# Kernel tuning notes

Hardware: AMD Instinct MI355X
Metric: run time of the kernel (lower is better)

Reference implementation:

```python
import jax, jax.numpy as jnp
import numpy as np

NEG_SLOPE = 0.2
EPS = 1e-16


def gat_layer(x, edge_index, edge_attr, W, We, a_src, a_dst, a_edge, bias,
              add_self_loops):
    """PyG GATConv with concat=True.
    x: [N, F_in], edge_index: [2, E] (row 0 = src j, row 1 = dst i),
    edge_attr: [E, De], W: [F_in, H*C], We: [De, H*C],
    a_src/a_dst/a_edge: [H, C], bias: [H*C].
    """
    N = x.shape[0]
    H, C = a_src.shape
    if add_self_loops:
        # fill_value='mean': self-loop edge_attr = mean of incoming edge_attr per node
        dst0 = edge_index[1]
        s = jax.ops.segment_sum(edge_attr, dst0, num_segments=N)
        cnt = jax.ops.segment_sum(jnp.ones((edge_attr.shape[0], 1), edge_attr.dtype),
                                  dst0, num_segments=N)
        loop_attr = s / jnp.maximum(cnt, 1.0)
        loop_idx = jnp.arange(N, dtype=edge_index.dtype)
        edge_index = jnp.concatenate(
            [edge_index, jnp.stack([loop_idx, loop_idx])], axis=1)
        edge_attr = jnp.concatenate([edge_attr, loop_attr], axis=0)

    src, dst = edge_index[0], edge_index[1]
    h = (x @ W).reshape(N, H, C)                       # [N, H, C]
    e = (edge_attr @ We).reshape(-1, H, C)             # [E, H, C]

    alpha_src = jnp.einsum('nhc,hc->nh', h, a_src)     # [N, H]
    alpha_dst = jnp.einsum('nhc,hc->nh', h, a_dst)     # [N, H]
    alpha_edge = jnp.einsum('ehc,hc->eh', e, a_edge)   # [E, H]

    alpha = alpha_src[src] + alpha_dst[dst] + alpha_edge
    alpha = jax.nn.leaky_relu(alpha, NEG_SLOPE)

    # segment softmax over destination node
    amax = jax.ops.segment_max(alpha, dst, num_segments=N)      # [N, H]
    ex = jnp.exp(alpha - amax[dst])
    denom = jax.ops.segment_sum(ex, dst, num_segments=N)        # [N, H]
    attn = ex / (denom[dst] + EPS)                               # [E, H]

    msg = h[src] * attn[:, :, None]                              # [E, H, C]
    out = jax.ops.segment_sum(msg, dst, num_segments=N)          # [N, H, C]
    return out.reshape(N, H * C) + bias


def setup_inputs() -> dict:
    key = jax.random.key(0)
    ks = jax.random.split(key, 16)
    N, E, F_in, C, H, De = 10000, 160000, 128, 64, 8, 1
    d1 = H * C  # 512

    def glorot(k, shape):
        fan = shape[0] + shape[-1]
        s = jnp.sqrt(6.0 / fan)
        return jax.random.uniform(k, shape, jnp.float32, -s, s)

    return {
        'x': jax.random.normal(ks[0], (N, F_in), jnp.float32),
        'edge_index': jax.random.randint(ks[1], (2, E), 0, N, jnp.int32),
        'edge_attr': jax.random.normal(ks[2], (E, De), jnp.float32),
        # layer 1 params
        'W1': glorot(ks[3], (F_in, d1)),
        'We1': glorot(ks[4], (De, d1)),
        'as1': glorot(ks[5], (H, C)),
        'ad1': glorot(ks[6], (H, C)),
        'ae1': glorot(ks[7], (H, C)),
        'b1': jnp.zeros((d1,), jnp.float32),
        # layer 2 params
        'W2': glorot(ks[8], (d1, d1)),
        'We2': glorot(ks[9], (De, d1)),
        'as2': glorot(ks[10], (H, C)),
        'ad2': glorot(ks[11], (H, C)),
        'ae2': glorot(ks[12], (H, C)),
        'b2': jnp.zeros((d1,), jnp.float32),
    }


def reference(x, edge_index, edge_attr,
              W1, We1, as1, ad1, ae1, b1,
              W2, We2, as2, ad2, ae2, b2):
    h = gat_layer(x, edge_index, edge_attr, W1, We1, as1, ad1, ae1, b1,
                  add_self_loops=False)
    h = jax.nn.relu(h)
    h = gat_layer(h, edge_index, edge_attr, W2, We2, as2, ad2, ae2, b2,
                  add_self_loops=True)
    return jnp.mean(h, axis=0)  # [512]
```

## Files before the change

kernel.cpp:

```cpp
#include <hip/hip_runtime.h>
#include <hip/hip_bf16.h>

#define HD __device__ __forceinline__
typedef unsigned short u16;
typedef __attribute__((ext_vector_type(8))) short bf16x8;
typedef __attribute__((ext_vector_type(4))) float f32x4;

HD u16 f2b(float f){
  unsigned u = __float_as_uint(f);
  unsigned r = (u + 0x7fffu + ((u>>16)&1u)) >> 16;
  return (u16)r;
}
HD float b2f(short s){ return __uint_as_float(((unsigned)(u16)s)<<16); }

__global__ void k_count(const int* __restrict__ dst, const float* __restrict__ ea,
                        int* cnt, float* easum, int E){
  int e = blockIdx.x*blockDim.x + threadIdx.x;
  if (e>=E) return;
  int d = dst[e];
  atomicAdd(&cnt[d],1);
  atomicAdd(&easum[d], ea[e]);
}

__global__ __launch_bounds__(1024) void k_scan(const int* __restrict__ cnt, int* offs, int N){
  __shared__ int lds[1024];
  const int chunk = (N + 1023)/1024;
  const int b = threadIdx.x*chunk;
  int s = 0;
  for (int i=0;i<chunk;++i){ int idx=b+i; if (idx<N) s += cnt[idx]; }
  lds[threadIdx.x] = s;
  __syncthreads();
  #pragma unroll
  for (int off=1; off<1024; off<<=1){
    int t = (threadIdx.x>=(unsigned)off)? lds[threadIdx.x-off] : 0;
    __syncthreads();
    lds[threadIdx.x] += t;
    __syncthreads();
  }
  int excl = lds[threadIdx.x] - s;
  for (int i=0;i<chunk;++i){
    int idx=b+i;
    if (idx<N){ offs[idx] = excl; excl += cnt[idx]; }
  }
  if (threadIdx.x==1023) offs[N] = lds[1023];
}

__global__ void k_scatter(const int* __restrict__ src, const int* __restrict__ dst,
                          const float* __restrict__ ea, const int* __restrict__ offs,
                          int* fill, int* srcs, float* eas, int E){
  int e = blockIdx.x*blockDim.x + threadIdx.x;
  if (e>=E) return;
  int d = dst[e];
  int p = offs[d] + atomicAdd(&fill[d],1);
  srcs[p] = src[e];
  eas[p]  = ea[e];
}

__global__ __launch_bounds__(512) void k_prep_small(
    const int* __restrict__ cnt, const float* __restrict__ easum, float* la, int N,
    const float* __restrict__ We1, const float* __restrict__ ae1,
    const float* __restrict__ We2, const float* __restrict__ ae2,
    float* wedot, int nbLoop){
  int bx = blockIdx.x;
  if (bx < nbLoop){
    int n = bx*512 + threadIdx.x;
    if (n<N) la[n] = easum[n] / fmaxf((float)cnt[n], 1.f);
    return;
  }
  int which = bx - nbLoop;
  const float* We = which? We2 : We1;
  const float* ae = which? ae2 : ae1;
  int hh = threadIdx.x>>6, lane = threadIdx.x&63;
  float p = We[hh*64+lane]*ae[hh*64+lane];
  #pragma unroll
  for (int o=32;o;o>>=1) p += __shfl_down(p,o);
  if (lane==0) wedot[which*8+hh] = p;
}

__global__ __launch_bounds__(256) void k_prep_cast(
    const float* __restrict__ x, u16* __restrict__ xb, int total4,
    const float* __restrict__ W1, u16* __restrict__ W1t,
    const float* __restrict__ W2, u16* __restrict__ W2t,
    int nbCast, int nbW1){
  __shared__ float T[64][65];
  int bx = blockIdx.x;
  if (bx < nbCast){
    int i = bx*256 + threadIdx.x;
    if (i<total4){
      float4 v = *(const float4*)(x + (size_t)i*4);
      ushort4 o; o.x=f2b(v.x); o.y=f2b(v.y); o.z=f2b(v.z); o.w=f2b(v.w);
      *(ushort4*)(xb + (size_t)i*4) = o;
    }
    return;
  }
  const float* W; u16* Wt; int K, Nn, t;
  if (bx < nbCast + nbW1){ t = bx - nbCast;        W = W1; Wt = W1t; K = 128; Nn = 512; }
  else                   { t = bx - nbCast - nbW1; W = W2; Wt = W2t; K = 512; Nn = 512; }
  int nt = Nn/64;
  int k0 = (t/nt)*64, n0 = (t%nt)*64;
  #pragma unroll
  for (int i=0;i<16;++i){
    int id = i*256 + threadIdx.x;
    int r = id>>6, c = id&63;
    T[r][c] = W[(size_t)(k0+r)*Nn + n0 + c];
  }
  __syncthreads();
  #pragma unroll
  for (int i=0;i<16;++i){
    int id = i*256 + threadIdx.x;
    int rr = id>>6, cc = id&63;
    Wt[(size_t)(n0+rr)*K + k0 + cc] = f2b(T[cc][rr]);
  }
}

__global__ __launch_bounds__(256) void k_gemm_mfma(
    const u16* __restrict__ A, const u16* __restrict__ Bt,
    u16* __restrict__ Cb, int M, int N, int K){
  __shared__ char lds[256*80];
  char* As = lds;
  char* Bs = lds + 128*80;
  const int tid = threadIdx.x;
  const int lane = tid & 63, w = tid >> 6;
  const int wr = w >> 1, wc = w & 1;
  const int l15 = lane & 15, l4 = lane >> 4;
  const int m0 = blockIdx.y*128, n0 = blockIdx.x*128;

  f32x4 acc[4][4] = {};
  int aoff[4], boff[4];
  #pragma unroll
  for (int i=0;i<4;++i) aoff[i] = (wr*64 + i*16 + l15)*80 + l4*16;
  #pragma unroll
  for (int j=0;j<4;++j) boff[j] = (wc*64 + j*16 + l15)*80 + l4*16;

  for (int k0=0; k0<K; k0+=32){
    #pragma unroll
    for (int i=0;i<2;++i){
      int cid = tid*2+i;
      int r = cid>>2, c = cid&3;
      int row = m0 + r;
      float4 v = make_float4(0.f,0.f,0.f,0.f);
      if (row < M) v = *(const float4*)(A + (size_t)row*K + k0 + c*8);
      *(float4*)(As + r*80 + c*16) = v;
    }
    #pragma unroll
    for (int i=0;i<2;++i){
      int cid = tid*2+i;
      int r = cid>>2, c = cid&3;
      float4 v = *(const float4*)(Bt + (size_t)(n0+r)*K + k0 + c*8);
      *(float4*)(Bs + r*80 + c*16) = v;
    }
    __syncthreads();
    bf16x8 a[4], b[4];
    #pragma unroll
    for (int i=0;i<4;++i) a[i] = *reinterpret_cast<const bf16x8*>(As + aoff[i]);
    #pragma unroll
    for (int j=0;j<4;++j) b[j] = *reinterpret_cast<const bf16x8*>(Bs + boff[j]);
    #pragma unroll
    for (int i=0;i<4;++i)
      #pragma unroll
      for (int j=0;j<4;++j)
        acc[i][j] = __builtin_amdgcn_mfma_f32_16x16x32_bf16(a[i], b[j], acc[i][j], 0,0,0);
    __syncthreads();
  }
  #pragma unroll
  for (int i=0;i<4;++i){
    #pragma unroll
    for (int j=0;j<4;++j){
      #pragma unroll
      for (int r=0;r<4;++r){
        int row = m0 + wr*64 + i*16 + l4*4 + r;
        int col = n0 + wc*64 + j*16 + l15;
        if (row < M) Cb[(size_t)row*N + col] = f2b(acc[i][j][r]);
      }
    }
  }
}

__global__ __launch_bounds__(256) void k_alpha_nodes(const u16* __restrict__ hb,
    const float* __restrict__ a_s, const float* __restrict__ a_d,
    float* asrc, float* adst, int N){
  int n = blockIdx.x*4 + (threadIdx.x>>6);
  if (n>=N) return;
  int lane = threadIdx.x&63;
  int c0 = lane*8;
  bf16x8 v = *(const bf16x8*)(hb + (size_t)n*512 + c0);
  float s = 0.f, d = 0.f;
  #pragma unroll
  for (int j=0;j<8;++j){
    float f = b2f(v[j]);
    s = fmaf(f, a_s[c0+j], s);
    d = fmaf(f, a_d[c0+j], d);
  }
  #pragma unroll
  for (int o=1;o<8;o<<=1){ s += __shfl_xor(s,o); d += __shfl_xor(d,o); }
  if ((lane&7)==0){ int hh = lane>>3; asrc[n*8+hh]=s; adst[n*8+hh]=d; }
}

__global__ __launch_bounds__(256) void k_flashagg(const u16* __restrict__ hb,
    const int* __restrict__ srcs, const float* __restrict__ eas,
    const int* __restrict__ offs,
    const float* __restrict__ asrc, const float* __restrict__ adst,
    const float* __restrict__ wedot, const float* __restrict__ la,
    const float* __restrict__ bias,
    u16* __restrict__ outb,
    int N, int relu_flag, int self_flag){
  int n = blockIdx.x*4 + (threadIdx.x>>6);
  if (n>=N) return;
  int lane = threadIdx.x&63;
  int hh = lane&7, esub = lane>>3;
  int ahh = lane>>3;
  int c0 = lane*8;
  int beg = offs[n], end = offs[n+1];
  float wd = wedot[hh];
  float adn = adst[n*8+hh];

  float aselfa = -1e30f;
  if (self_flag){
    float a = asrc[n*8+hh] + adn + la[n]*wd;
    aselfa = a>0.f ? a : 0.2f*a;
  }
  float aself_c = __shfl(aselfa, ahh);

  float m = self_flag ? aself_c : -1e30f;
  float s = 0.f;
  float acc[8] = {};

  for (int p0=beg; p0<end; p0+=8){
    int p = p0 + esub;
    float a = -1e30f;
    if (p < end){
      int sp = srcs[p];
      a = asrc[sp*8+hh] + adn + eas[p]*wd;
      a = a>0.f ? a : 0.2f*a;
    }
    float av[8];
    #pragma unroll
    for (int e=0;e<8;++e) av[e] = __shfl(a, e*8 + ahh);
    float mo = m;
    #pragma unroll
    for (int e=0;e<8;++e) mo = fmaxf(mo, av[e]);
    float f = __expf(m - mo);
    m = mo;
    s *= f;
    #pragma unroll
    for (int j=0;j<8;++j) acc[j] *= f;
    #pragma unroll
    for (int e=0;e<8;++e){
      if (p0 + e < end){
        int se = srcs[p0+e];
        float ee = __expf(av[e] - m);
        s += ee;
        bf16x8 v = *(const bf16x8*)(hb + (size_t)se*512 + c0);
        #pragma unroll
        for (int j=0;j<8;++j) acc[j] = fmaf(ee, b2f(v[j]), acc[j]);
      }
    }
  }
  if (self_flag){
    float xs = __expf(aself_c - m);
    s += xs;
    bf16x8 v = *(const bf16x8*)(hb + (size_t)n*512 + c0);
    #pragma unroll
    for (int j=0;j<8;++j) acc[j] = fmaf(xs, b2f(v[j]), acc[j]);
  }
  float iv = 1.f/(s + 1e-16f);
  bf16x8 ov;
  #pragma unroll
  for (int j=0;j<8;++j){
    float val = acc[j]*iv + bias[c0+j];
    if (relu_flag) val = fmaxf(val, 0.f);
    ov[j] = (short)f2b(val);
  }
  *(bf16x8*)(outb + (size_t)n*512 + c0) = ov;
}

__global__ __launch_bounds__(512) void k_colmean(const u16* __restrict__ out2b,
                          float* __restrict__ o, int N, float invN){
  int c = threadIdx.x;
  int n0 = blockIdx.x*16;
  int nend = min(n0+16, N);
  float s = 0.f;
  for (int n=n0;n<nend;++n) s += b2f(out2b[(size_t)n*512 + c]);
  atomicAdd(&o[c], s*invN);
}

extern "C" void kernel_launch(void* const* d_in, const int* in_sizes, int n_in,
                              void* d_out, int out_size, void* d_ws, size_t ws_size,
                              hipStream_t stream){
  const float* x   = (const float*)d_in[0];
  const int* eidx  = (const int*)d_in[1];
  const float* ea  = (const float*)d_in[2];
  const float* W1  = (const float*)d_in[3];
  const float* We1 = (const float*)d_in[4];
  const float* as1 = (const float*)d_in[5];
  const float* ad1 = (const float*)d_in[6];
  const float* ae1 = (const float*)d_in[7];
  const float* b1  = (const float*)d_in[8];
  const float* W2  = (const float*)d_in[9];
  const float* We2 = (const float*)d_in[10];
  const float* as2 = (const float*)d_in[11];
  const float* ad2 = (const float*)d_in[12];
  const float* ae2 = (const float*)d_in[13];
  const float* b2  = (const float*)d_in[14];
  float* outp = (float*)d_out;

  const int FIN = 128, D1 = 512;
  const int N = in_sizes[0]/FIN;
  const int E = in_sizes[1]/2;
  const int* srcA = eidx;
  const int* dstA = eidx + E;

  char* ws = (char*)d_ws;
  size_t o = 0;
  auto alloc = [&](size_t bytes)->void*{
    void* p = ws + o; o = (o + bytes + 255) & ~(size_t)255; return p;
  };
  u16*   hb1   = (u16*)  alloc((size_t)N*D1*2);
  u16*   hb2   = (u16*)  alloc((size_t)N*D1*2);
  u16*   out1rb= (u16*)  alloc((size_t)N*D1*2);
  u16*   out2b = (u16*)  alloc((size_t)N*D1*2);
  u16*   xb    = (u16*)  alloc((size_t)N*FIN*2);
  u16*   W1t   = (u16*)  alloc((size_t)D1*FIN*2);
  u16*   W2t   = (u16*)  alloc((size_t)D1*D1*2);
  int*   srcs  = (int*)  alloc((size_t)E*4);
  float* eas   = (float*)alloc((size_t)E*4);
  int*   offs  = (int*)  alloc((size_t)(N+1)*4);
  size_t zbeg = o;
  int*   cnt   = (int*)  alloc((size_t)N*4);
  int*   fill  = (int*)  alloc((size_t)N*4);
  float* easum = (float*)alloc((size_t)N*4);
  size_t zend = o;
  float* asrc  = (float*)alloc((size_t)N*8*4);
  float* adst  = (float*)alloc((size_t)N*8*4);
  float* la    = (float*)alloc((size_t)N*4);
  float* wedot = (float*)alloc(64);
  (void)ws_size; (void)n_in;

  hipMemsetAsync(ws + zbeg, 0, zend - zbeg, stream);
  hipMemsetAsync(d_out, 0, (size_t)out_size*sizeof(float), stream);

  dim3 b256(256);
  int ge = (E+255)/256;
  int gn4 = (N+3)/4;

  k_count   <<<ge, b256, 0, stream>>>(dstA, ea, cnt, easum, E);
  k_scan    <<<1, 1024, 0, stream>>>(cnt, offs, N);
  k_scatter <<<ge, b256, 0, stream>>>(srcA, dstA, ea, offs, fill, srcs, eas, E);
  {
    int nbLoop = (N+511)/512;
    k_prep_small<<<nbLoop+2, 512, 0, stream>>>(cnt, easum, la, N,
                                               We1, ae1, We2, ae2, wedot, nbLoop);
    int total4 = N*FIN/4;
    int nbCast = (total4+255)/256;
    int nbW1 = (FIN/64)*(D1/64);
    int nbW2 = (D1/64)*(D1/64);
    k_prep_cast<<<nbCast+nbW1+nbW2, b256, 0, stream>>>(x, xb, total4,
                                                       W1, W1t, W2, W2t, nbCast, nbW1);
  }

  k_gemm_mfma<<<dim3(D1/128, (N+127)/128), b256, 0, stream>>>(xb, W1t, hb1, N, D1, FIN);
  k_alpha_nodes<<<gn4, b256, 0, stream>>>(hb1, as1, ad1, asrc, adst, N);
  k_flashagg<<<gn4, b256, 0, stream>>>(hb1, srcs, eas, offs, asrc, adst, wedot, la,
                                       b1, out1rb, N, 1, 0);

  k_gemm_mfma<<<dim3(D1/128, (N+127)/128), b256, 0, stream>>>(out1rb, W2t, hb2, N, D1, D1);
  k_alpha_nodes<<<gn4, b256, 0, stream>>>(hb2, as2, ad2, asrc, adst, N);
  k_flashagg<<<gn4, b256, 0, stream>>>(hb2, srcs, eas, offs, asrc, adst, wedot+8, la,
                                       b2, out2b, N, 0, 1);

  k_colmean<<<(N+15)/16, 512, 0, stream>>>(out2b, outp, N, 1.0f/(float)N);
}
```

Before: 187.6 us.

## Fuse attention logit dot products into GEMM epilogue and widen aggregation batch

```diff
diff --git a/kernel.cpp b/kernel.cpp
--- a/kernel.cpp
+++ b/kernel.cpp
@@ -115,7 +115,10 @@
 
 __global__ __launch_bounds__(256) void k_gemm_mfma(
     const u16* __restrict__ A, const u16* __restrict__ Bt,
-    u16* __restrict__ Cb, int M, int N, int K){
+    u16* __restrict__ Cb,
+    const float* __restrict__ a_s, const float* __restrict__ a_d,
+    float* __restrict__ asrc, float* __restrict__ adst,
+    int M, int N, int K){
   __shared__ char lds[256*80];
   char* As = lds;
   char* Bs = lds + 128*80;
@@ -162,38 +165,42 @@
         acc[i][j] = __builtin_amdgcn_mfma_f32_16x16x32_bf16(a[i], b[j], acc[i][j], 0,0,0);
     __syncthreads();
   }
+
+  const int head = (n0>>6) + wc;
+  float sv[4][4] = {}, dv[4][4] = {};
   #pragma unroll
   for (int i=0;i<4;++i){
     #pragma unroll
     for (int j=0;j<4;++j){
+      int col = n0 + wc*64 + j*16 + l15;
+      float asv = a_s[col], adv = a_d[col];
       #pragma unroll
       for (int r=0;r<4;++r){
         int row = m0 + wr*64 + i*16 + l4*4 + r;
-        int col = n0 + wc*64 + j*16 + l15;
-        if (row < M) Cb[(size_t)row*N + col] = f2b(acc[i][j][r]);
+        u16 bits = f2b(acc[i][j][r]);
+        float valf = b2f((short)bits);
+        if (row < M) Cb[(size_t)row*N + col] = bits;
+        sv[i][r] = fmaf(valf, asv, sv[i][r]);
+        dv[i][r] = fmaf(valf, adv, dv[i][r]);
       }
     }
   }
-}
-
-__global__ __launch_bounds__(256) void k_alpha_nodes(const u16* __restrict__ hb,
-    const float* __restrict__ a_s, const float* __restrict__ a_d,
-    float* asrc, float* adst, int N){
-  int n = blockIdx.x*4 + (threadIdx.x>>6);
-  if (n>=N) return;
-  int lane = threadIdx.x&63;
-  int c0 = lane*8;
-  bf16x8 v = *(const bf16x8*)(hb + (size_t)n*512 + c0);
-  float s = 0.f, d = 0.f;
-  #pragma unroll
-  for (int j=0;j<8;++j){
-    float f = b2f(v[j]);
-    s = fmaf(f, a_s[c0+j], s);
-    d = fmaf(f, a_d[c0+j], d);
-  }
-  #pragma unroll
-  for (int o=1;o<8;o<<=1){ s += __shfl_xor(s,o); d += __shfl_xor(d,o); }
-  if ((lane&7)==0){ int hh = lane>>3; asrc[n*8+hh]=s; adst[n*8+hh]=d; }
+  #pragma unroll
+  for (int i=0;i<4;++i){
+    #pragma unroll
+    for (int r=0;r<4;++r){
+      float s_ = sv[i][r], d_ = dv[i][r];
+      #pragma unroll
+      for (int mask=1; mask<16; mask<<=1){
+        s_ += __shfl_xor(s_, mask);
+        d_ += __shfl_xor(d_, mask);
+      }
+      if (l15==0){
+        int row = m0 + wr*64 + i*16 + l4*4 + r;
+        if (row < M){ asrc[row*8+head] = s_; adst[row*8+head] = d_; }
+      }
+    }
+  }
 }
 
 __global__ __launch_bounds__(256) void k_flashagg(const u16* __restrict__ hb,
@@ -225,32 +232,41 @@
   float s = 0.f;
   float acc[8] = {};
 
-  for (int p0=beg; p0<end; p0+=8){
-    int p = p0 + esub;
-    float a = -1e30f;
-    if (p < end){
-      int sp = srcs[p];
-      a = asrc[sp*8+hh] + adn + eas[p]*wd;
-      a = a>0.f ? a : 0.2f*a;
-    }
-    float av[8];
-    #pragma unroll
-    for (int e=0;e<8;++e) av[e] = __shfl(a, e*8 + ahh);
+  for (int p0=beg; p0<end; p0+=16){
+    int pA = p0 + esub, pB = p0 + 8 + esub;
+    float aA = -1e30f, aB = -1e30f;
+    int sA = 0, sB = 0;
+    if (pA < end){
+      sA = srcs[pA];
+      float eaA = eas[pA];
+      float a = asrc[sA*8+hh] + adn + eaA*wd;
+      aA = a>0.f ? a : 0.2f*a;
+    }
+    if (pB < end){
+      sB = srcs[pB];
+      float eaB = eas[pB];
+      float a = asrc[sB*8+hh] + adn + eaB*wd;
+      aB = a>0.f ? a : 0.2f*a;
+    }
+    float av[16]; int se[16];
+    #pragma unroll
+    for (int e=0;e<8;++e){ av[e]   = __shfl(aA, e*8 + ahh); se[e]   = __shfl(sA, e*8); }
+    #pragma unroll
+    for (int e=0;e<8;++e){ av[8+e] = __shfl(aB, e*8 + ahh); se[8+e] = __shfl(sB, e*8); }
     float mo = m;
     #pragma unroll
-    for (int e=0;e<8;++e) mo = fmaxf(mo, av[e]);
+    for (int e=0;e<16;++e) mo = fmaxf(mo, av[e]);
     float f = __expf(m - mo);
     m = mo;
     s *= f;
     #pragma unroll
     for (int j=0;j<8;++j) acc[j] *= f;
     #pragma unroll
-    for (int e=0;e<8;++e){
+    for (int e=0;e<16;++e){
       if (p0 + e < end){
-        int se = srcs[p0+e];
         float ee = __expf(av[e] - m);
         s += ee;
-        bf16x8 v = *(const bf16x8*)(hb + (size_t)se*512 + c0);
+        bf16x8 v = *(const bf16x8*)(hb + (size_t)se[e]*512 + c0);
         #pragma unroll
         for (int j=0;j<8;++j) acc[j] = fmaf(ee, b2f(v[j]), acc[j]);
       }
@@ -358,13 +374,13 @@
                                                        W1, W1t, W2, W2t, nbCast, nbW1);
   }
 
-  k_gemm_mfma<<<dim3(D1/128, (N+127)/128), b256, 0, stream>>>(xb, W1t, hb1, N, D1, FIN);
-  k_alpha_nodes<<<gn4, b256, 0, stream>>>(hb1, as1, ad1, asrc, adst, N);
+  k_gemm_mfma<<<dim3(D1/128, (N+127)/128), b256, 0, stream>>>(
+      xb, W1t, hb1, as1, ad1, asrc, adst, N, D1, FIN);
   k_flashagg<<<gn4, b256, 0, stream>>>(hb1, srcs, eas, offs, asrc, adst, wedot, la,
                                        b1, out1rb, N, 1, 0);
 
-  k_gemm_mfma<<<dim3(D1/128, (N+127)/128), b256, 0, stream>>>(out1rb, W2t, hb2, N, D1, D1);
-  k_alpha_nodes<<<gn4, b256, 0, stream>>>(hb2, as2, ad2, asrc, adst, N);
+  k_gemm_mfma<<<dim3(D1/128, (N+127)/128), b256, 0, stream>>>(
+      out1rb, W2t, hb2, as2, ad2, asrc, adst, N, D1, D1);
   k_flashagg<<<gn4, b256, 0, stream>>>(hb2, srcs, eas, offs, asrc, adst, wedot+8, la,
                                        b2, out2b, N, 0, 1);
 
```

New measurement: 179.8 us. 1.04x faster.
